# Performance work log

Measured on AMD Instinct MI355X. Metric: run time of the kernel, lower is better.

Reference implementation:

```python
import jax, jax.numpy as jnp
import numpy as np
from math import sqrt

B, T, C = 4, 2048, 2048
H = 16
D = C // H  # head_dim = 128


def setup_inputs() -> dict:
    key = jax.random.key(0)
    ks = jax.random.split(key, 7)
    s = 1.0 / sqrt(C)
    return {
        "querys": jax.random.normal(ks[0], (B, T, C), dtype=jnp.float32),
        "keys": jax.random.normal(ks[1], (B, T, C), dtype=jnp.float32),
        "values": jax.random.normal(ks[2], (B, T, C), dtype=jnp.float32),
        "Wq": jax.random.normal(ks[3], (C, C), dtype=jnp.float32) * s,
        "bq": jnp.zeros((C,), dtype=jnp.float32),
        "Wk": jax.random.normal(ks[4], (C, C), dtype=jnp.float32) * s,
        "bk": jnp.zeros((C,), dtype=jnp.float32),
        "Wv": jax.random.normal(ks[5], (C, C), dtype=jnp.float32) * s,
        "bv": jnp.zeros((C,), dtype=jnp.float32),
        "Wo": jax.random.normal(ks[6], (C, C), dtype=jnp.float32) * s,
        "bo": jnp.zeros((C,), dtype=jnp.float32),
        "is_causal": 1,
    }


def reference(querys, keys, values, Wq, bq, Wk, bk, Wv, bv, Wo, bo, is_causal):
    # Linear projections: x @ W^T + b (torch nn.Linear convention), here W stored as [C_in, C_out]
    q = (querys @ Wq + bq).reshape(B, T, H, D)
    k = (keys @ Wk + bk).reshape(B, T, H, D)
    v = (values @ Wv + bv).reshape(B, T, H, D)
    # scores: [B, H, T, T]
    scores = jnp.einsum("bqhd,bkhd->bhqk", q, k) / sqrt(D)
    if is_causal:
        mask = jnp.tril(jnp.ones((T, T), dtype=bool))  # allowed positions
        scores = jnp.where(mask, scores, -jnp.inf)
    weights = jax.nn.softmax(scores, axis=-1)
    attn = jnp.einsum("bhqk,bkhd->bqhd", weights, v).reshape(B, T, C)
    return attn @ Wo + bo
```

## Files before the change

kernel.cpp:

```cpp
#include <hip/hip_runtime.h>
#include <hip/hip_bf16.h>
#include <stdint.h>

#define BB 4
#define TT 2048
#define CC 2048
#define HH 16
#define DD 128
#define MM (BB*TT)

typedef __attribute__((ext_vector_type(8))) short bh8;
typedef __attribute__((ext_vector_type(4))) float fx4;

__device__ inline ushort f2bf(float x) {
    union { float f; uint32_t u; } c; c.f = x;
    uint32_t lsb = (c.u >> 16) & 1u;
    return (ushort)((c.u + 0x7fffu + lsb) >> 16);
}

__device__ inline void async16(const void* g, void* l) {
    __builtin_amdgcn_global_load_lds(
        (const __attribute__((address_space(1))) uint32_t*)g,
        (__attribute__((address_space(3))) uint32_t*)l, 16, 0, 0);
}

__global__ __launch_bounds__(256) void convert3_k(
    const float* __restrict__ i0, const float* __restrict__ i1,
    const float* __restrict__ i2,
    ushort* __restrict__ o0, ushort* __restrict__ o1, ushort* __restrict__ o2,
    int n)
{
    const float* in; ushort* out;
    switch (blockIdx.y) {
        case 0:  in = i0; out = o0; break;
        case 1:  in = i1; out = o1; break;
        default: in = i2; out = o2; break;
    }
    int i = (int)(blockIdx.x * 256 + threadIdx.x) * 4;
    if (i + 3 < n) {
        float4 v = *(const float4*)&in[i];
        ushort4 o;
        o.x = f2bf(v.x); o.y = f2bf(v.y); o.z = f2bf(v.z); o.w = f2bf(v.w);
        *(ushort4*)&out[i] = o;
    }
}

__global__ __launch_bounds__(256) void transpose4_w_k(
    const float* __restrict__ w0, const float* __restrict__ w1,
    const float* __restrict__ w2, const float* __restrict__ w3,
    ushort* __restrict__ t0, ushort* __restrict__ t1,
    ushort* __restrict__ t2, ushort* __restrict__ t3)
{
    const float* W; ushort* Wt;
    switch (blockIdx.z) {
        case 0:  W = w0; Wt = t0; break;
        case 1:  W = w1; Wt = t1; break;
        case 2:  W = w2; Wt = t2; break;
        default: W = w3; Wt = t3; break;
    }
    __shared__ __align__(16) ushort tile[32][33];
    const int n0 = blockIdx.x * 32, k0 = blockIdx.y * 32;
    const int tx = threadIdx.x, ty = threadIdx.y;
#pragma unroll
    for (int r = 0; r < 32; r += 8)
        tile[ty + r][tx] = f2bf(W[(size_t)(k0 + ty + r) * CC + n0 + tx]);
    __syncthreads();
    const int tid = ty * 32 + tx;
    const int p = tid & 15;
    const int row = tid >> 4;
#pragma unroll
    for (int rr = 0; rr < 2; ++rr) {
        const int n_row = row + rr * 16;
        ushort2 w2;
        w2.x = tile[2 * p][n_row];
        w2.y = tile[2 * p + 1][n_row];
        *(ushort2*)&Wt[(size_t)(n0 + n_row) * CC + k0 + 2 * p] = w2;
    }
}

__global__ __launch_bounds__(256) void transpose_v_k(
    const ushort* __restrict__ V, ushort* __restrict__ Vt)
{
    __shared__ __align__(16) ushort tile[32][33];
    const int bh = blockIdx.z;
    const int b = bh >> 4, h = bh & 15;
    const int t0 = blockIdx.y * 32, d0 = blockIdx.x * 32;
    const int tx = threadIdx.x, ty = threadIdx.y;
    const ushort* Vp = V + (size_t)b * TT * CC + h * DD;
#pragma unroll
    for (int r = 0; r < 32; r += 8)
        tile[ty + r][tx] = Vp[(size_t)(t0 + ty + r) * CC + d0 + tx];
    __syncthreads();
    ushort* Vtp = Vt + (size_t)bh * DD * TT;
    const int tt = t0 + tx;
    const int pnew = (tt & ~31) | (((tt >> 2) & 3) << 3) | (((tt >> 4) & 1) << 2) | (tt & 3);
#pragma unroll
    for (int r = 0; r < 32; r += 8)
        Vtp[(size_t)(d0 + ty + r) * TT + pnew] = tile[tx][ty + r];
}

template<int OUTF>
__global__ __launch_bounds__(512, 2) void gemm_bf16_k(
    const ushort* __restrict__ A, const ushort* __restrict__ Bt,
    const float* __restrict__ bias, void* __restrict__ Cv, float osc)
{
    __shared__ __align__(16) char Gsm[2][65536];

    const int tid = (int)threadIdx.x;
    const int lane = tid & 63, wave = tid >> 6;
    const int fr = lane & 15, fg = lane >> 4;
    const int wm = wave >> 2, wn = wave & 3;

    const int bid = (int)blockIdx.x;
    const int xcd = bid & 7, local = bid >> 3;
    const int m_tile = xcd * 4 + (local >> 3);
    const int n_tile = local & 7;
    const int m0 = m_tile * 256, n0 = n_tile * 256;

    const ushort* Ag = A  + (size_t)m0 * CC;
    const ushort* Bg = Bt + (size_t)n0 * CC;
    const int nt = CC / 64;

    auto STAGE_G = [&](int t, int g) {
        if (t >= nt) return;
        const int khalf = g >> 1, isB = g & 1;
        char* base = Gsm[t & 1] + isB * 32768 + khalf * 16384;
        const ushort* src = isB ? Bg : Ag;
        const int kbase = t * 64 + khalf * 32;
#pragma unroll
        for (int l = 0; l < 2; ++l) {
            const int u = l * 512 + tid;
            const int j = u >> 3, s = u & 7;
            const int ek = s ^ (j & 7);
            const int e = (ek >> 2) & 1, ks = ek & 3;
            async16(src + (size_t)(2 * j + e) * CC + kbase + ks * 8,
                    base + u * 16);
        }
    };

    const int slot = ((((fr & 1) << 2) | fg) ^ ((fr >> 1) & 7));
    const int offA = (wm * 64 + (fr >> 1)) * 128 + slot * 16;
    const int offB = 32768 + (wn * 32 + (fr >> 1)) * 128 + slot * 16;

    fx4 acc[8][4];
#pragma unroll
    for (int i = 0; i < 8; ++i)
#pragma unroll
        for (int j = 0; j < 4; ++j)
            acc[i][j] = (fx4){0.f, 0.f, 0.f, 0.f};

#pragma unroll
    for (int g = 0; g < 4; ++g) STAGE_G(0, g);

#pragma unroll 1
    for (int t = 0; t < nt; ++t) {
        const char* kb = Gsm[t & 1];
#pragma unroll
        for (int kk = 0; kk < 2; ++kk) {
            if (t == nt - 1 && kk == 1) {
                asm volatile("s_waitcnt vmcnt(0)" ::: "memory");
            } else {
                asm volatile("s_waitcnt vmcnt(4)" ::: "memory");
            }
            __builtin_amdgcn_sched_barrier(0);
            __builtin_amdgcn_s_barrier();
            __builtin_amdgcn_sched_barrier(0);

            const char* ka = kb + kk * 16384;
            const char* kbB = kb + kk * 16384;
            bh8 afr[4], bfr[4];

#pragma unroll
            for (int nf = 0; nf < 4; ++nf)
                bfr[nf] = *(const bh8*)(kbB + offB + nf * 1024);
#pragma unroll
            for (int i = 0; i < 4; ++i)
                afr[i] = *(const bh8*)(ka + offA + i * 1024);
            STAGE_G(t + 1, kk * 2);

            __builtin_amdgcn_sched_barrier(0);
            __builtin_amdgcn_s_barrier();
            __builtin_amdgcn_sched_barrier(0);

            __builtin_amdgcn_s_setprio(1);
#pragma unroll
            for (int i = 0; i < 4; ++i)
#pragma unroll
                for (int nf = 0; nf < 4; ++nf)
                    acc[i][nf] = __builtin_amdgcn_mfma_f32_16x16x32_bf16(
                        afr[i], bfr[nf], acc[i][nf], 0, 0, 0);
            __builtin_amdgcn_s_setprio(0);

#pragma unroll
            for (int i = 0; i < 4; ++i)
                afr[i] = *(const bh8*)(ka + offA + (4 + i) * 1024);
            STAGE_G(t + 1, kk * 2 + 1);

            __builtin_amdgcn_sched_barrier(0);
            __builtin_amdgcn_s_barrier();
            __builtin_amdgcn_sched_barrier(0);

            __builtin_amdgcn_s_setprio(1);
#pragma unroll
            for (int i = 0; i < 4; ++i)
#pragma unroll
                for (int nf = 0; nf < 4; ++nf)
                    acc[4 + i][nf] = __builtin_amdgcn_mfma_f32_16x16x32_bf16(
                        afr[i], bfr[nf], acc[4 + i][nf], 0, 0, 0);
            __builtin_amdgcn_s_setprio(0);
        }
    }

#pragma unroll
    for (int nf = 0; nf < 4; ++nf) {
        const int col = n0 + wn * 64 + nf * 16 + fr;
        const float bv = bias[col];
#pragma unroll
        for (int mf = 0; mf < 8; ++mf) {
            const int row = m0 + wm * 128 + mf * 16 + fg * 4;
#pragma unroll
            for (int r = 0; r < 4; ++r) {
                float v = (acc[mf][nf][r] + bv) * osc;
                if (OUTF)
                    ((float*)Cv)[(size_t)(row + r) * CC + col] = v;
                else
                    ((ushort*)Cv)[(size_t)(row + r) * CC + col] = f2bf(v);
            }
        }
    }
}

__global__ __launch_bounds__(512, 4) void flash_attn_k(
    const ushort* __restrict__ Qm, const ushort* __restrict__ Km,
    const ushort* __restrict__ Vt, ushort* __restrict__ Om,
    const int* __restrict__ causal_p)
{
    __shared__ __align__(16) char Ksm[2][16384];
    __shared__ __align__(16) char Vsm[2][16384];

    const int tid = (int)threadIdx.x;
    const int lane = tid & 63, wave = tid >> 6;
    const int fr = lane & 15, fg = lane >> 4;
    const int causal = causal_p[0];

    const int d_raw = (int)blockIdx.x + 8 * ((int)blockIdx.y + 16 * (int)blockIdx.z);
    const int xcd = d_raw & 7, jj = d_raw >> 3;
    const int head_lin = xcd * 8 + (jj & 7);
    const int pi = jj >> 3;
    const int h = head_lin & 15, b = head_lin >> 4;

    const ushort* Qp = Qm + (size_t)b * TT * CC + h * DD;
    const ushort* Kp = Km + (size_t)b * TT * CC + h * DD;
    const ushort* Vp = Vt + (size_t)(b * HH + h) * DD * TT;
    ushort* Op = Om + (size_t)b * TT * CC + h * DD;

    const bh8 onesf = {0x3F80, 0x3F80, 0x3F80, 0x3F80,
                       0x3F80, 0x3F80, 0x3F80, 0x3F80};

    auto STAGE = [&](int ti, int buf) {
        const int kv0 = ti * 64;
        {
            const int r0 = tid >> 4, s0 = tid & 15;
            async16(Kp + (size_t)(kv0 + r0) * CC + (s0 ^ (r0 & 15)) * 8,
                    Ksm[buf] + tid * 16);
            async16(Kp + (size_t)(kv0 + 32 + r0) * CC + (s0 ^ (r0 & 15)) * 8,
                    Ksm[buf] + 8192 + tid * 16);
        }
        {
            const int d0 = tid >> 3, s0 = tid & 7;
            async16(Vp + (size_t)d0 * TT + kv0 + (s0 ^ (d0 & 7)) * 8,
                    Vsm[buf] + tid * 16);
            async16(Vp + (size_t)(64 + d0) * TT + kv0 + (s0 ^ (d0 & 7)) * 8,
                    Vsm[buf] + 8192 + tid * 16);
        }
    };

#pragma unroll 1
    for (int pp = 0; pp < 2; ++pp) {
        const int tile = pp ? (15 - pi) : pi;
        const int q0 = tile * 128;
        const int qbase = q0 + wave * 16;
        const int q_idx = qbase + fr;

        bh8 qf[4];
#pragma unroll
        for (int s = 0; s < 4; ++s)
            qf[s] = *(const bh8*)&Qp[(size_t)(qbase + fr) * CC + s * 32 + fg * 8];

        fx4 o[8];
#pragma unroll
        for (int jn = 0; jn < 8; ++jn) o[jn] = (fx4){0.f, 0.f, 0.f, 0.f};
        fx4 o_l = (fx4){0.f, 0.f, 0.f, 0.f};

        const int nfull  = causal ? (q0 >> 6) : (TT / 64);
        const int ntiles = causal ? (nfull + 2) : (TT / 64);

        STAGE(0, 0);
#pragma unroll 1
        for (int t = 0; t < ntiles; ++t) {
            const bool last = (t == ntiles - 1);
            if (!last) STAGE(t + 1, (t + 1) & 1);
            if (!last) { asm volatile("s_waitcnt vmcnt(4)" ::: "memory"); }
            else       { asm volatile("s_waitcnt vmcnt(0)" ::: "memory"); }
            __builtin_amdgcn_sched_barrier(0);
            __builtin_amdgcn_s_barrier();
            __builtin_amdgcn_sched_barrier(0);

            const int kv0 = t * 64;
            const char* kb = Ksm[t & 1];
            const char* vb = Vsm[t & 1];
            const bool domask = causal && (t >= nfull);
            const bool active = !domask || (kv0 <= qbase + 15);

            if (active) {
                fx4 s4[4];
#pragma unroll
                for (int j = 0; j < 4; ++j) s4[j] = (fx4){0.f, 0.f, 0.f, 0.f};
                __builtin_amdgcn_s_setprio(1);
#pragma unroll
                for (int st = 0; st < 4; ++st) {
                    bh8 kf[4];
#pragma unroll
                    for (int j = 0; j < 4; ++j)
                        kf[j] = *(const bh8*)(kb + (j * 16 + fr) * 256 +
                                              ((st * 64 + fg * 16) ^ (fr << 4)));
#pragma unroll
                    for (int j = 0; j < 4; ++j)
                        s4[j] = __builtin_amdgcn_mfma_f32_16x16x32_bf16(
                            kf[j], qf[st], s4[j], 0, 0, 0);
                }
                __builtin_amdgcn_s_setprio(0);

#pragma unroll
                for (int g = 0; g < 2; ++g) {
                    float pg[2][4];
#pragma unroll
                    for (int j2 = 0; j2 < 2; ++j2) {
                        const int jb = g * 2 + j2;
#pragma unroll
                        for (int r = 0; r < 4; ++r) {
                            float v = s4[jb][r];
                            if (domask && (kv0 + jb * 16 + fg * 4 + r > q_idx))
                                v = -1e30f;
                            pg[j2][r] = exp2f(v);
                        }
                    }
                    union { uint u[4]; bh8 h; } pk;
                    asm("v_cvt_pk_bf16_f32 %0, %1, %2"
                        : "=v"(pk.u[0]) : "v"(pg[0][0]), "v"(pg[0][1]));
                    asm("v_cvt_pk_bf16_f32 %0, %1, %2"
                        : "=v"(pk.u[1]) : "v"(pg[0][2]), "v"(pg[0][3]));
                    asm("v_cvt_pk_bf16_f32 %0, %1, %2"
                        : "=v"(pk.u[2]) : "v"(pg[1][0]), "v"(pg[1][1]));
                    asm("v_cvt_pk_bf16_f32 %0, %1, %2"
                        : "=v"(pk.u[3]) : "v"(pg[1][2]), "v"(pg[1][3]));
                    const bh8 pf = pk.h;

                    o_l = __builtin_amdgcn_mfma_f32_16x16x32_bf16(
                        pf, onesf, o_l, 0, 0, 0);

                    __builtin_amdgcn_s_setprio(1);
#pragma unroll
                    for (int jn = 0; jn < 8; ++jn) {
                        bh8 vf = *(const bh8*)(vb + (jn * 16 + fr) * 128 +
                                               ((g * 64 + fg * 16) ^ ((fr & 7) << 4)));
                        o[jn] = __builtin_amdgcn_mfma_f32_16x16x32_bf16(
                            pf, vf, o[jn], 0, 0, 0);
                    }
                    __builtin_amdgcn_s_setprio(0);
                }
            }

            __builtin_amdgcn_sched_barrier(0);
            __builtin_amdgcn_s_barrier();
            __builtin_amdgcn_sched_barrier(0);
        }

#pragma unroll
        for (int r = 0; r < 4; ++r) {
            const float inv = 1.0f / o_l[r];
            const size_t rowoff = (size_t)(qbase + fg * 4 + r) * CC;
#pragma unroll
            for (int jn = 0; jn < 8; ++jn)
                Op[rowoff + jn * 16 + fr] = f2bf(o[jn][r] * inv);
        }
    }
}

extern "C" void kernel_launch(void* const* d_in, const int* in_sizes, int n_in,
                              void* d_out, int out_size, void* d_ws, size_t ws_size,
                              hipStream_t stream)
{
    (void)in_sizes; (void)n_in; (void)out_size;
    const float* querys = (const float*)d_in[0];
    const float* keys   = (const float*)d_in[1];
    const float* values = (const float*)d_in[2];
    const float* Wq = (const float*)d_in[3];
    const float* bq = (const float*)d_in[4];
    const float* Wk = (const float*)d_in[5];
    const float* bk = (const float*)d_in[6];
    const float* Wv = (const float*)d_in[7];
    const float* bv = (const float*)d_in[8];
    const float* Wo = (const float*)d_in[9];
    const float* bo = (const float*)d_in[10];
    const int* is_causal = (const int*)d_in[11];

    const size_t WBYTES = (size_t)CC * CC * 2;
    const size_t XBYTES = (size_t)MM * CC * 2;
    if (ws_size < 4 * WBYTES + 4 * XBYTES) return;

    uint8_t* ws = (uint8_t*)d_ws;
    ushort* WqT = (ushort*)(ws);
    ushort* WkT = (ushort*)(ws + WBYTES);
    ushort* WvT = (ushort*)(ws + 2 * WBYTES);
    ushort* WoT = (ushort*)(ws + 3 * WBYTES);
    uint8_t* act = ws + 4 * WBYTES;
    ushort* Xq = (ushort*)(act);
    ushort* Xk = (ushort*)(act + XBYTES);
    ushort* Xv = (ushort*)(act + 2 * XBYTES);
    ushort* Qb = (ushort*)(act + 3 * XBYTES);
    ushort* Kb = Xq;
    ushort* Vb = Xk;
    ushort* Vt = Xv;
    ushort* Ob = Xk;

    dim3 tb(32, 8);
    transpose4_w_k<<<dim3(CC / 32, CC / 32, 4), tb, 0, stream>>>(
        Wq, Wk, Wv, Wo, WqT, WkT, WvT, WoT);

    const int nX = MM * CC;
    convert3_k<<<dim3(nX / 4 / 256, 3), 256, 0, stream>>>(
        querys, keys, values, Xq, Xk, Xv, nX);

    dim3 gg((MM / 256) * (CC / 256));

    const float QSC = 0.12751789836306614f;

    gemm_bf16_k<0><<<gg, 512, 0, stream>>>(Xq, WqT, bq, Qb, QSC);
    gemm_bf16_k<0><<<gg, 512, 0, stream>>>(Xk, WkT, bk, Kb, 1.0f);
    gemm_bf16_k<0><<<gg, 512, 0, stream>>>(Xv, WvT, bv, Vb, 1.0f);

    dim3 gvt(DD / 32, TT / 32, BB * HH);
    transpose_v_k<<<gvt, tb, 0, stream>>>(Vb, Vt);

    dim3 ga(8, HH, BB);
    flash_attn_k<<<ga, 512, 0, stream>>>(Qb, Kb, Vt, Ob, is_causal);

    gemm_bf16_k<1><<<gg, 512, 0, stream>>>(Ob, WoT, bo, d_out, 1.0f);
}
```

Measured before the change: 456.8 us.

## Batch QKV GEMMs into one launch and use one barrier per attention tile

The three Q/K/V projection GEMMs now run as a single launch, with blockIdx.y choosing the operands. This cuts launch gaps and lets blocks from different projections fill the GPU together, which may help the tail. In the flash-attention loop, each iteration now waits for all outstanding loads and hits one barrier at the top, then prefetches the next K/V tile into the other buffer. This removes the barrier at the end of the tile. The catch is that the load wait now happens before compute starts instead of after the next prefetch is issued.

```diff
diff --git a/kernel.cpp b/kernel.cpp
--- a/kernel.cpp
+++ b/kernel.cpp
@@ -100,9 +100,8 @@
 }
 
 template<int OUTF>
-__global__ __launch_bounds__(512, 2) void gemm_bf16_k(
-    const ushort* __restrict__ A, const ushort* __restrict__ Bt,
-    const float* __restrict__ bias, void* __restrict__ Cv, float osc)
+__device__ __forceinline__ void gemm_body(
+    const ushort* A, const ushort* Bt, const float* bias, void* Cv, float osc)
 {
     __shared__ __align__(16) char Gsm[2][65536];
 
@@ -228,6 +227,32 @@
             }
         }
     }
+}
+
+__global__ __launch_bounds__(512, 2) void gemm_qkv_k(
+    const ushort* __restrict__ Xq, const ushort* __restrict__ Xk,
+    const ushort* __restrict__ Xv,
+    const ushort* __restrict__ WqT, const ushort* __restrict__ WkT,
+    const ushort* __restrict__ WvT,
+    const float* __restrict__ bq, const float* __restrict__ bk,
+    const float* __restrict__ bv,
+    ushort* __restrict__ Qb, ushort* __restrict__ Kb, ushort* __restrict__ Vb)
+{
+    const ushort* A; const ushort* Bt; const float* bias; ushort* Cv; float osc;
+    switch (blockIdx.y) {
+        case 0:  A = Xq; Bt = WqT; bias = bq; Cv = Qb;
+                 osc = 0.12751789836306614f; break;
+        case 1:  A = Xk; Bt = WkT; bias = bk; Cv = Kb; osc = 1.0f; break;
+        default: A = Xv; Bt = WvT; bias = bv; Cv = Vb; osc = 1.0f; break;
+    }
+    gemm_body<0>(A, Bt, bias, Cv, osc);
+}
+
+__global__ __launch_bounds__(512, 2) void gemm_o_k(
+    const ushort* __restrict__ A, const ushort* __restrict__ Bt,
+    const float* __restrict__ bias, float* __restrict__ Cv)
+{
+    gemm_body<1>(A, Bt, bias, Cv, 1.0f);
 }
 
 __global__ __launch_bounds__(512, 4) void flash_attn_k(
@@ -298,13 +323,11 @@
         STAGE(0, 0);
 #pragma unroll 1
         for (int t = 0; t < ntiles; ++t) {
-            const bool last = (t == ntiles - 1);
-            if (!last) STAGE(t + 1, (t + 1) & 1);
-            if (!last) { asm volatile("s_waitcnt vmcnt(4)" ::: "memory"); }
-            else       { asm volatile("s_waitcnt vmcnt(0)" ::: "memory"); }
+            asm volatile("s_waitcnt vmcnt(0)" ::: "memory");
             __builtin_amdgcn_sched_barrier(0);
             __builtin_amdgcn_s_barrier();
             __builtin_amdgcn_sched_barrier(0);
+            if (t + 1 < ntiles) STAGE(t + 1, (t + 1) & 1);
 
             const int kv0 = t * 64;
             const char* kb = Ksm[t & 1];
@@ -370,10 +393,6 @@
                     __builtin_amdgcn_s_setprio(0);
                 }
             }
-
-            __builtin_amdgcn_sched_barrier(0);
-            __builtin_amdgcn_s_barrier();
-            __builtin_amdgcn_sched_barrier(0);
         }
 
 #pragma unroll
@@ -432,13 +451,8 @@
     convert3_k<<<dim3(nX / 4 / 256, 3), 256, 0, stream>>>(
         querys, keys, values, Xq, Xk, Xv, nX);
 
-    dim3 gg((MM / 256) * (CC / 256));
-
-    const float QSC = 0.12751789836306614f;
-
-    gemm_bf16_k<0><<<gg, 512, 0, stream>>>(Xq, WqT, bq, Qb, QSC);
-    gemm_bf16_k<0><<<gg, 512, 0, stream>>>(Xk, WkT, bk, Kb, 1.0f);
-    gemm_bf16_k<0><<<gg, 512, 0, stream>>>(Xv, WvT, bv, Vb, 1.0f);
+    gemm_qkv_k<<<dim3((MM / 256) * (CC / 256), 3), 512, 0, stream>>>(
+        Xq, Xk, Xv, WqT, WkT, WvT, bq, bk, bv, Qb, Kb, Vb);
 
     dim3 gvt(DD / 32, TT / 32, BB * HH);
     transpose_v_k<<<gvt, tb, 0, stream>>>(Vb, Vt);
@@ -446,5 +460,6 @@
     dim3 ga(8, HH, BB);
     flash_attn_k<<<ga, 512, 0, stream>>>(Qb, Kb, Vt, Ob, is_causal);
 
-    gemm_bf16_k<1><<<gg, 512, 0, stream>>>(Ob, WoT, bo, d_out, 1.0f);
-}
+    gemm_o_k<<<dim3((MM / 256) * (CC / 256)), 512, 0, stream>>>(
+        Ob, WoT, bo, (float*)d_out);
+}
```

Result: faster. 447.2 us (-2.1%).
